# Kernel tuning notes

Hardware: AMD Instinct MI355X
Metric: run time of the kernel (lower is better)

## Reference

```python
import jax, jax.numpy as jnp
import numpy as np

REL_SIZE = 65
TAG_SIZE = 4


def _rope(y):
    # Interleaved rotary position embedding, matching the torch module:
    # cos_pos = cos(theta) repeat_interleave(2), sin_pos = sin(theta) repeat_interleave(2)
    # y2 = (-y1, y0, -y3, y2, ...)
    B, S, H = y.shape
    half = H // 2
    pos = jnp.arange(S, dtype=jnp.float32)[:, None]                      # (S,1)
    inv_freq = jnp.power(10000.0, -2.0 * jnp.arange(half, dtype=jnp.float32) / H)
    theta = pos * inv_freq                                               # (S, half)
    cos = jnp.repeat(jnp.cos(theta), 2, axis=-1)                          # (S, H)
    sin = jnp.repeat(jnp.sin(theta), 2, axis=-1)                          # (S, H)
    yr = y.reshape(B, S, half, 2)
    y2 = jnp.stack([-yr[..., 1], yr[..., 0]], axis=-1).reshape(B, S, H)
    return y * cos + y2 * sin


def setup_inputs() -> dict:
    key = jax.random.key(0)
    k1, k2, k3 = jax.random.split(key, 3)
    B, S, H = 1, 160, 768
    y = jax.random.normal(k1, (B, S, H), dtype=jnp.float32)
    event_idx = jax.random.randint(k2, (B, 16), 0, S)
    W1 = jax.random.normal(k3, (H, 2 * H), dtype=jnp.float32) * 0.02
    b1 = jnp.zeros((H,), dtype=jnp.float32)
    W2 = jax.random.normal(jax.random.fold_in(key, 7), (REL_SIZE * TAG_SIZE, H), dtype=jnp.float32) * 0.02
    b2 = jnp.zeros((REL_SIZE * TAG_SIZE,), dtype=jnp.float32)
    return {"y": y, "event_idx": event_idx, "W1": W1, "b1": b1, "W2": W2, "b2": b2}


def reference(y, event_idx, W1, b1, W2, b2):
    # Eval path (training=False): event_idx unused, dropout = identity, sigmoid applied.
    B, S, H = y.shape
    yrot = _rope(y)
    # Linear(cat(a, b)) is separable: split W1 into the halves acting on a and b.
    Wa, Wb = W1[:, :H], W1[:, H:]
    left = jnp.einsum('bsh,oh->bso', yrot, Wa)                  # contribution of token i (row)
    right = jnp.einsum('bsh,oh->bso', yrot, Wb) + b1            # contribution of token j (col)
    h = jax.nn.relu(left[:, :, None, :] + right[:, None, :, :])  # (B, S, S, H)
    out = jnp.einsum('bijh,oh->bijo', h, W2) + b2               # (B, S, S, 260)
    out = out.reshape(B, S, S, REL_SIZE, TAG_SIZE).transpose(0, 3, 1, 2, 4)  # (B, 65, S, S, 4)
    return jax.nn.sigmoid(out)
```

## Files before the change

### kernel.cpp

```cpp
#include <hip/hip_runtime.h>
#include <hip/hip_bf16.h>
#include <cstdint>

#define SDIM 160
#define HDIM 768
#define HALF 384
#define ODIM 260
#define OPAD 272
#define CHUNK_BYTES 34816
#define WS_SMALL 1155088
#define WS_BIG   3514384

typedef __attribute__((ext_vector_type(8))) short short8;
typedef __attribute__((ext_vector_type(4))) float floatx4;
typedef _Float16 half8 __attribute__((ext_vector_type(8)));

typedef const __attribute__((address_space(1))) unsigned char gl_u8;
typedef __attribute__((address_space(3))) unsigned char lds_u8;

static __device__ __forceinline__ float bf2f(unsigned short u) {
    union { unsigned int i; float f; } v; v.i = ((unsigned int)u) << 16; return v.f;
}
static __device__ __forceinline__ unsigned short f2bf(float x) {
    __hip_bfloat16 h = __float2bfloat16(x);
    return *reinterpret_cast<unsigned short*>(&h);
}
static __device__ __forceinline__ unsigned short f2h(float x) {
    _Float16 h = (_Float16)x;
    return *reinterpret_cast<unsigned short*>(&h);
}
static __device__ __forceinline__ float q(float x) { return bf2f(f2bf(x)); }

__global__ __launch_bounds__(256) void prep_kernel(
    const float* __restrict__ y, const float* __restrict__ W1,
    const float* __restrict__ W2,
    unsigned short* __restrict__ yb, unsigned short* __restrict__ W2b,
    unsigned short* __restrict__ W1b, int do_w1b) {
    int bid = blockIdx.x;
    int t = threadIdx.x;
    if (bid < SDIM) {
        int s = bid;
        for (int p = t; p < HALF; p += 256) {
            float invf = __expf(-(2.0f * (float)p / (float)HDIM) * 9.210340371976184f);
            float th = (float)s * invf;
            float c = cosf(th), sn = sinf(th);
            float y0 = y[s * HDIM + 2 * p], y1 = y[s * HDIM + 2 * p + 1];
            yb[s * HDIM + 2 * p]     = f2bf(y0 * c - y1 * sn);
            yb[s * HDIM + 2 * p + 1] = f2bf(y1 * c + y0 * sn);
        }
    } else if (bid < SDIM + 102) {
        int idx = (bid - SDIM) * 256 + t;
        if (idx < 96 * OPAD) {
            int kg = idx % 96, row = idx / 96;
            unsigned short o8[8];
            if (row < ODIM) {
                float4 a = *reinterpret_cast<const float4*>(W2 + row * HDIM + kg * 8);
                float4 b = *reinterpret_cast<const float4*>(W2 + row * HDIM + kg * 8 + 4);
                o8[0] = f2h(a.x); o8[1] = f2h(a.y); o8[2] = f2h(a.z); o8[3] = f2h(a.w);
                o8[4] = f2h(b.x); o8[5] = f2h(b.y); o8[6] = f2h(b.z); o8[7] = f2h(b.w);
            } else {
                #pragma unroll
                for (int e = 0; e < 8; ++e) o8[e] = 0;
            }
            *reinterpret_cast<uint4*>(W2b + ((size_t)kg * OPAD + row) * 8) =
                *reinterpret_cast<uint4*>(o8);
        }
    } else if (do_w1b) {
        int idx = (bid - SDIM - 102) * 256 + t;
        int kg = idx % 96, row = idx / 96;
        const float* src = (row < 768) ? (W1 + row * 1536 + kg * 8)
                                       : (W1 + (row - 768) * 1536 + 768 + kg * 8);
        float4 a = *reinterpret_cast<const float4*>(src);
        float4 b = *reinterpret_cast<const float4*>(src + 4);
        unsigned short o8[8];
        o8[0] = f2bf(a.x); o8[1] = f2bf(a.y); o8[2] = f2bf(a.z); o8[3] = f2bf(a.w);
        o8[4] = f2bf(b.x); o8[5] = f2bf(b.y); o8[6] = f2bf(b.z); o8[7] = f2bf(b.w);
        *reinterpret_cast<uint4*>(W1b + ((size_t)kg * 1536 + row) * 8) =
            *reinterpret_cast<uint4*>(o8);
    }
}

__global__ __launch_bounds__(64, 2) void lr3_kernel(
    const unsigned short* __restrict__ yb, const unsigned short* __restrict__ W1b,
    const float* __restrict__ b1,
    unsigned short* __restrict__ Lb, unsigned short* __restrict__ Rt) {
    int l = threadIdx.x & 63;
    int l16 = l & 15, qd = l >> 4;
    int mtb = blockIdx.x * 4;
    int sp = blockIdx.y;
    int s0 = sp * 32 + l16;
    int s1 = s0 + 16;

    floatx4 acc[2][4];
    #pragma unroll
    for (int st = 0; st < 2; ++st)
        #pragma unroll
        for (int mtl = 0; mtl < 4; ++mtl)
            acc[st][mtl] = (floatx4){0.0f, 0.0f, 0.0f, 0.0f};

    const unsigned short* yrow0 = yb + s0 * HDIM;
    const unsigned short* yrow1 = yb + s1 * HDIM;

    for (int ks = 0; ks < 24; ++ks) {
        int k = ks * 32 + qd * 8;
        int kg = ks * 4 + qd;
        union { uint4 u; short8 s; } bu0, bu1;
        bu0.u = *reinterpret_cast<const uint4*>(yrow0 + k);
        bu1.u = *reinterpret_cast<const uint4*>(yrow1 + k);
        #pragma unroll
        for (int mtl = 0; mtl < 4; ++mtl) {
            union { uint4 u; short8 s; } au;
            au.u = *reinterpret_cast<const uint4*>(
                W1b + ((size_t)kg * 1536 + (mtb + mtl) * 16 + l16) * 8);
            acc[0][mtl] = __builtin_amdgcn_mfma_f32_16x16x32_bf16(
                au.s, bu0.s, acc[0][mtl], 0, 0, 0);
            acc[1][mtl] = __builtin_amdgcn_mfma_f32_16x16x32_bf16(
                au.s, bu1.s, acc[1][mtl], 0, 0, 0);
        }
    }

    #pragma unroll
    for (int st = 0; st < 2; ++st) {
        int s_out = sp * 32 + st * 16 + l16;
        #pragma unroll
        for (int mtl = 0; mtl < 4; ++mtl) {
            int o2 = (mtb + mtl) * 16 + qd * 4;
            unsigned short out4[4];
            if (o2 < 768) {
                #pragma unroll
                for (int r = 0; r < 4; ++r) out4[r] = f2h(acc[st][mtl][r]);
                *reinterpret_cast<uint2*>(Lb + s_out * HDIM + o2) =
                    *reinterpret_cast<uint2*>(out4);
            } else {
                int ob = o2 - 768;
                #pragma unroll
                for (int r = 0; r < 4; ++r)
                    out4[r] = f2h(acc[st][mtl][r] + b1[ob + r]);
                *reinterpret_cast<uint2*>(
                    Rt + ((size_t)(ob >> 3) * SDIM + s_out) * 8 + (ob & 7)) =
                    *reinterpret_cast<uint2*>(out4);
            }
        }
    }
}

__global__ __launch_bounds__(256) void lr_fallback_kernel(
    const unsigned short* __restrict__ yb, const float* __restrict__ W1,
    const float* __restrict__ b1,
    unsigned short* __restrict__ Lb, unsigned short* __restrict__ Rt) {
    int idx = blockIdx.x * 256 + threadIdx.x;
    int s = idx / 1536;
    int o2 = idx - s * 1536;
    const unsigned short* yrow = yb + s * HDIM;
    if (o2 < 768) {
        const float* wp = W1 + o2 * 1536;
        float a0 = 0.0f;
        for (int k = 0; k < HDIM; ++k) a0 += q(wp[k]) * bf2f(yrow[k]);
        Lb[s * HDIM + o2] = f2h(a0);
    } else {
        int ob = o2 - 768;
        const float* wp = W1 + ob * 1536 + 768;
        float a0 = 0.0f;
        for (int k = 0; k < HDIM; ++k) a0 += q(wp[k]) * bf2f(yrow[k]);
        Rt[((size_t)(ob >> 3) * SDIM + s) * 8 + (ob & 7)] = f2h(a0 + b1[ob]);
    }
}

__global__ __launch_bounds__(512) void main_kernel(
    const unsigned short* __restrict__ Lb, const unsigned short* __restrict__ Rt,
    const unsigned short* __restrict__ W2b,
    const float* __restrict__ b2, float* __restrict__ out) {
    __shared__ __align__(16) unsigned char lds[2 * CHUNK_BYTES];

    int w = threadIdx.x >> 6;
    int l = threadIdx.x & 63;
    int l16 = l & 15, qd = l >> 4;
    int jh = w & 1;
    int mq = w >> 1;
    int mt0 = mq * 4;
    int nmt = (mq == 3) ? 5 : 4;
    int i0 = blockIdx.x * 2;
    int j = blockIdx.y * 32 + jh * 16 + l16;

    floatx4 acc[2][5];
    #pragma unroll
    for (int c = 0; c < 2; ++c)
        #pragma unroll
        for (int mtl = 0; mtl < 5; ++mtl)
            acc[c][mtl] = (floatx4){0.0f, 0.0f, 0.0f, 0.0f};

    const unsigned short* Lrow0 = Lb + i0 * HDIM;
    const unsigned short* Lrow1 = Lb + (i0 + 1) * HDIM;
    const unsigned char* wsrc = reinterpret_cast<const unsigned char*>(W2b);

    #pragma unroll
    for (int it = 0; it < 5; ++it) {
        int seg = w + it * 8;
        if (seg < 34) {
            __builtin_amdgcn_global_load_lds(
                (gl_u8*)(wsrc + seg * 1024 + l * 16),
                (lds_u8*)(lds + seg * 1024), 16, 0, 0);
        }
    }
    __syncthreads();

    for (int kc = 0; kc < 12; ++kc) {
        int buf = kc & 1;
        if (kc < 11) {
            const unsigned char* gsrc = wsrc + (kc + 1) * CHUNK_BYTES;
            unsigned char* ldst = lds + (1 - buf) * CHUNK_BYTES;
            #pragma unroll
            for (int it = 0; it < 5; ++it) {
                int seg = w + it * 8;
                if (seg < 34) {
                    __builtin_amdgcn_global_load_lds(
                        (gl_u8*)(gsrc + seg * 1024 + l * 16),
                        (lds_u8*)(ldst + seg * 1024), 16, 0, 0);
                }
            }
        }
        #pragma unroll
        for (int ks = 0; ks < 2; ++ks) {
            int k = kc * 64 + ks * 32 + qd * 8;
            int kg = kc * 8 + ks * 4 + qd;
            half8 bfrag[2];
            union { uint4 u; half8 h; } ru;
            ru.u = *reinterpret_cast<const uint4*>(
                Rt + ((size_t)kg * SDIM + j) * 8);
            #pragma unroll
            for (int c = 0; c < 2; ++c) {
                const unsigned short* Lr = c ? Lrow1 : Lrow0;
                union { uint4 u; half8 h; } lu;
                lu.u = *reinterpret_cast<const uint4*>(Lr + k);
                half8 hv = lu.h + ru.h;
                #pragma unroll
                for (int e = 0; e < 8; ++e)
                    hv[e] = hv[e] > (_Float16)0.0f ? hv[e] : (_Float16)0.0f;
                bfrag[c] = hv;
            }
            int ldsbase = buf * CHUNK_BYTES + ((ks * 4 + qd) * OPAD + l16) * 16;
            #pragma unroll
            for (int mtl = 0; mtl < 5; ++mtl) {
                if (mtl < nmt) {
                    union { uint4 u; half8 h; } au;
                    au.u = *reinterpret_cast<const uint4*>(
                        lds + ldsbase + (mt0 + mtl) * 256);
                    acc[0][mtl] = __builtin_amdgcn_mfma_f32_16x16x32_f16(
                        au.h, bfrag[0], acc[0][mtl], 0, 0, 0);
                    acc[1][mtl] = __builtin_amdgcn_mfma_f32_16x16x32_f16(
                        au.h, bfrag[1], acc[1][mtl], 0, 0, 0);
                }
            }
        }
        __syncthreads();
    }

    #pragma unroll
    for (int c = 0; c < 2; ++c) {
        int i = i0 + c;
        #pragma unroll
        for (int mtl = 0; mtl < 5; ++mtl) {
            if (mtl < nmt) {
                int ob = (mt0 + mtl) * 16 + qd * 4;
                if (ob < ODIM) {
                    float4 bv = *reinterpret_cast<const float4*>(b2 + ob);
                    int rel = ob >> 2;
                    float4 v;
                    v.x = 1.0f / (1.0f + __expf(-(acc[c][mtl][0] + bv.x)));
                    v.y = 1.0f / (1.0f + __expf(-(acc[c][mtl][1] + bv.y)));
                    v.z = 1.0f / (1.0f + __expf(-(acc[c][mtl][2] + bv.z)));
                    v.w = 1.0f / (1.0f + __expf(-(acc[c][mtl][3] + bv.w)));
                    *reinterpret_cast<float4*>(
                        out + (((rel * SDIM) + i) * SDIM + j) * 4) = v;
                }
            }
        }
    }
}

__global__ void ws_too_small_kernel(float* out) { out[0] = 999.0f; }

extern "C" void kernel_launch(void* const* d_in, const int* in_sizes, int n_in,
                              void* d_out, int out_size, void* d_ws, size_t ws_size,
                              hipStream_t stream) {
    const float* y  = (const float*)d_in[0];
    const float* W1 = (const float*)d_in[2];
    const float* b1 = (const float*)d_in[3];
    const float* W2 = (const float*)d_in[4];
    const float* b2 = (const float*)d_in[5];
    float* out = (float*)d_out;

    if (ws_size < (size_t)WS_SMALL) {
        ws_too_small_kernel<<<dim3(1), dim3(1), 0, stream>>>(out);
        return;
    }

    unsigned short* yb  = (unsigned short*)((char*)d_ws + 16);
    unsigned short* Lb  = yb + SDIM * HDIM;
    unsigned short* Rt  = Lb + SDIM * HDIM;
    unsigned short* W2b = Rt + SDIM * HDIM;
    unsigned short* W1b = W2b + 96 * OPAD * 8;

    if (ws_size >= (size_t)WS_BIG) {
        prep_kernel<<<dim3(SDIM + 102 + 576), dim3(256), 0, stream>>>(
            y, W1, W2, yb, W2b, W1b, 1);
        lr3_kernel<<<dim3(24, 5), dim3(64), 0, stream>>>(yb, W1b, b1, Lb, Rt);
        main_kernel<<<dim3(80, 5), dim3(512), 0, stream>>>(Lb, Rt, W2b, b2, out);
    } else {
        prep_kernel<<<dim3(SDIM + 102), dim3(256), 0, stream>>>(
            y, W1, W2, yb, W2b, W1b, 0);
        lr_fallback_kernel<<<dim3(960), dim3(256), 0, stream>>>(yb, W1, b1, Lb, Rt);
        main_kernel<<<dim3(80, 5), dim3(512), 0, stream>>>(Lb, Rt, W2b, b2, out);
    }
}
```

Before: 118.9 us.

## Fuse prep and LR GEMM into one cooperative kernel with grid sync

Merges the RoPE/W2-conversion prep kernel and the L/R projection GEMM into a single cooperative kernel of 120 single-wave blocks separated by a grid-wide sync. W1 is no longer pre-converted to a bf16 workspace; each GEMM block reads fp32 W1 directly and converts it in registers. This removes one kernel launch and the W1b write/read round trip, at the cost of a grid barrier, far fewer threads doing the prep work, and uncoalesced fp32 W1 loads inside the MFMA loop.

Measured after the change: 178.2 us. 1.5x slower.

```diff
diff --git a/kernel.cpp b/kernel.cpp
--- a/kernel.cpp
+++ b/kernel.cpp
@@ -1,5 +1,6 @@
 #include <hip/hip_runtime.h>
 #include <hip/hip_bf16.h>
+#include <hip/hip_cooperative_groups.h>
 #include <cstdint>
 
 #define SDIM 160
@@ -8,8 +9,7 @@
 #define ODIM 260
 #define OPAD 272
 #define CHUNK_BYTES 34816
-#define WS_SMALL 1155088
-#define WS_BIG   3514384
+#define WS_NEED 1155088
 
 typedef __attribute__((ext_vector_type(8))) short short8;
 typedef __attribute__((ext_vector_type(4))) float floatx4;
@@ -18,6 +18,8 @@
 typedef const __attribute__((address_space(1))) unsigned char gl_u8;
 typedef __attribute__((address_space(3))) unsigned char lds_u8;
 
+namespace cg = cooperative_groups;
+
 static __device__ __forceinline__ float bf2f(unsigned short u) {
     union { unsigned int i; float f; } v; v.i = ((unsigned int)u) << 16; return v.f;
 }
@@ -29,29 +31,37 @@
     _Float16 h = (_Float16)x;
     return *reinterpret_cast<unsigned short*>(&h);
 }
-static __device__ __forceinline__ float q(float x) { return bf2f(f2bf(x)); }
-
-__global__ __launch_bounds__(256) void prep_kernel(
+
+__global__ __launch_bounds__(64, 2) void fused_pre_lr_kernel(
     const float* __restrict__ y, const float* __restrict__ W1,
-    const float* __restrict__ W2,
+    const float* __restrict__ b1, const float* __restrict__ W2,
     unsigned short* __restrict__ yb, unsigned short* __restrict__ W2b,
-    unsigned short* __restrict__ W1b, int do_w1b) {
+    unsigned short* __restrict__ Lb, unsigned short* __restrict__ Rt) {
     int bid = blockIdx.x;
-    int t = threadIdx.x;
-    if (bid < SDIM) {
-        int s = bid;
-        for (int p = t; p < HALF; p += 256) {
-            float invf = __expf(-(2.0f * (float)p / (float)HDIM) * 9.210340371976184f);
-            float th = (float)s * invf;
-            float c = cosf(th), sn = sinf(th);
-            float y0 = y[s * HDIM + 2 * p], y1 = y[s * HDIM + 2 * p + 1];
-            yb[s * HDIM + 2 * p]     = f2bf(y0 * c - y1 * sn);
-            yb[s * HDIM + 2 * p + 1] = f2bf(y1 * c + y0 * sn);
-        }
-    } else if (bid < SDIM + 102) {
-        int idx = (bid - SDIM) * 256 + t;
-        if (idx < 96 * OPAD) {
-            int kg = idx % 96, row = idx / 96;
+    int l = threadIdx.x;
+    int gid = bid * 64 + l;
+
+    #pragma unroll
+    for (int it = 0; it < 8; ++it) {
+        int e = gid + it * 7680;
+        int s = e / 384;
+        int p = e - s * 384;
+        float invf = __expf(-(2.0f * (float)p / (float)HDIM) * 9.210340371976184f);
+        float th = (float)s * invf;
+        float c = cosf(th), sn = sinf(th);
+        float2 y2 = *reinterpret_cast<const float2*>(y + s * HDIM + 2 * p);
+        unsigned short r0 = f2bf(y2.x * c - y2.y * sn);
+        unsigned short r1 = f2bf(y2.y * c + y2.x * sn);
+        unsigned int pk = (unsigned int)r0 | ((unsigned int)r1 << 16);
+        *reinterpret_cast<unsigned int*>(yb + s * HDIM + 2 * p) = pk;
+    }
+
+    #pragma unroll
+    for (int it = 0; it < 4; ++it) {
+        int slot = gid + it * 7680;
+        if (slot < 96 * OPAD) {
+            int kg = slot / OPAD;
+            int row = slot - kg * OPAD;
             unsigned short o8[8];
             if (row < ODIM) {
                 float4 a = *reinterpret_cast<const float4*>(W2 + row * HDIM + kg * 8);
@@ -65,29 +75,13 @@
             *reinterpret_cast<uint4*>(W2b + ((size_t)kg * OPAD + row) * 8) =
                 *reinterpret_cast<uint4*>(o8);
         }
-    } else if (do_w1b) {
-        int idx = (bid - SDIM - 102) * 256 + t;
-        int kg = idx % 96, row = idx / 96;
-        const float* src = (row < 768) ? (W1 + row * 1536 + kg * 8)
-                                       : (W1 + (row - 768) * 1536 + 768 + kg * 8);
-        float4 a = *reinterpret_cast<const float4*>(src);
-        float4 b = *reinterpret_cast<const float4*>(src + 4);
-        unsigned short o8[8];
-        o8[0] = f2bf(a.x); o8[1] = f2bf(a.y); o8[2] = f2bf(a.z); o8[3] = f2bf(a.w);
-        o8[4] = f2bf(b.x); o8[5] = f2bf(b.y); o8[6] = f2bf(b.z); o8[7] = f2bf(b.w);
-        *reinterpret_cast<uint4*>(W1b + ((size_t)kg * 1536 + row) * 8) =
-            *reinterpret_cast<uint4*>(o8);
-    }
-}
-
-__global__ __launch_bounds__(64, 2) void lr3_kernel(
-    const unsigned short* __restrict__ yb, const unsigned short* __restrict__ W1b,
-    const float* __restrict__ b1,
-    unsigned short* __restrict__ Lb, unsigned short* __restrict__ Rt) {
-    int l = threadIdx.x & 63;
+    }
+
+    cg::this_grid().sync();
+
     int l16 = l & 15, qd = l >> 4;
-    int mtb = blockIdx.x * 4;
-    int sp = blockIdx.y;
+    int mtb = (bid % 24) * 4;
+    int sp = bid / 24;
     int s0 = sp * 32 + l16;
     int s1 = s0 + 16;
 
@@ -109,9 +103,19 @@
         bu1.u = *reinterpret_cast<const uint4*>(yrow1 + k);
         #pragma unroll
         for (int mtl = 0; mtl < 4; ++mtl) {
+            int row = (mtb + mtl) * 16 + l16;
+            const float* src = (row < 768)
+                ? (W1 + (size_t)row * 1536 + kg * 8)
+                : (W1 + (size_t)(row - 768) * 1536 + 768 + kg * 8);
+            float4 wa = *reinterpret_cast<const float4*>(src);
+            float4 wb = *reinterpret_cast<const float4*>(src + 4);
+            unsigned short w8[8];
+            w8[0] = f2bf(wa.x); w8[1] = f2bf(wa.y);
+            w8[2] = f2bf(wa.z); w8[3] = f2bf(wa.w);
+            w8[4] = f2bf(wb.x); w8[5] = f2bf(wb.y);
+            w8[6] = f2bf(wb.z); w8[7] = f2bf(wb.w);
             union { uint4 u; short8 s; } au;
-            au.u = *reinterpret_cast<const uint4*>(
-                W1b + ((size_t)kg * 1536 + (mtb + mtl) * 16 + l16) * 8);
+            au.u = *reinterpret_cast<uint4*>(w8);
             acc[0][mtl] = __builtin_amdgcn_mfma_f32_16x16x32_bf16(
                 au.s, bu0.s, acc[0][mtl], 0, 0, 0);
             acc[1][mtl] = __builtin_amdgcn_mfma_f32_16x16x32_bf16(
@@ -141,28 +145,6 @@
                     *reinterpret_cast<uint2*>(out4);
             }
         }
-    }
-}
-
-__global__ __launch_bounds__(256) void lr_fallback_kernel(
-    const unsigned short* __restrict__ yb, const float* __restrict__ W1,
-    const float* __restrict__ b1,
-    unsigned short* __restrict__ Lb, unsigned short* __restrict__ Rt) {
-    int idx = blockIdx.x * 256 + threadIdx.x;
-    int s = idx / 1536;
-    int o2 = idx - s * 1536;
-    const unsigned short* yrow = yb + s * HDIM;
-    if (o2 < 768) {
-        const float* wp = W1 + o2 * 1536;
-        float a0 = 0.0f;
-        for (int k = 0; k < HDIM; ++k) a0 += q(wp[k]) * bf2f(yrow[k]);
-        Lb[s * HDIM + o2] = f2h(a0);
-    } else {
-        int ob = o2 - 768;
-        const float* wp = W1 + ob * 1536 + 768;
-        float a0 = 0.0f;
-        for (int k = 0; k < HDIM; ++k) a0 += q(wp[k]) * bf2f(yrow[k]);
-        Rt[((size_t)(ob >> 3) * SDIM + s) * 8 + (ob & 7)] = f2h(a0 + b1[ob]);
     }
 }
 
@@ -290,7 +272,7 @@
     const float* b2 = (const float*)d_in[5];
     float* out = (float*)d_out;
 
-    if (ws_size < (size_t)WS_SMALL) {
+    if (ws_size < (size_t)WS_NEED) {
         ws_too_small_kernel<<<dim3(1), dim3(1), 0, stream>>>(out);
         return;
     }
@@ -299,17 +281,10 @@
     unsigned short* Lb  = yb + SDIM * HDIM;
     unsigned short* Rt  = Lb + SDIM * HDIM;
     unsigned short* W2b = Rt + SDIM * HDIM;
-    unsigned short* W1b = W2b + 96 * OPAD * 8;
-
-    if (ws_size >= (size_t)WS_BIG) {
-        prep_kernel<<<dim3(SDIM + 102 + 576), dim3(256), 0, stream>>>(
-            y, W1, W2, yb, W2b, W1b, 1);
-        lr3_kernel<<<dim3(24, 5), dim3(64), 0, stream>>>(yb, W1b, b1, Lb, Rt);
-        main_kernel<<<dim3(80, 5), dim3(512), 0, stream>>>(Lb, Rt, W2b, b2, out);
-    } else {
-        prep_kernel<<<dim3(SDIM + 102), dim3(256), 0, stream>>>(
-            y, W1, W2, yb, W2b, W1b, 0);
-        lr_fallback_kernel<<<dim3(960), dim3(256), 0, stream>>>(yb, W1, b1, Lb, Rt);
-        main_kernel<<<dim3(80, 5), dim3(512), 0, stream>>>(Lb, Rt, W2b, b2, out);
-    }
-}
+
+    void* args[] = {(void*)&y, (void*)&W1, (void*)&b1, (void*)&W2,
+                    (void*)&yb, (void*)&W2b, (void*)&Lb, (void*)&Rt};
+    hipLaunchCooperativeKernel((const void*)fused_pre_lr_kernel,
+                               dim3(120), dim3(64), args, 0, stream);
+    main_kernel<<<dim3(80, 5), dim3(512), 0, stream>>>(Lb, Rt, W2b, b2, out);
+}
```
